# Kernel optimization log

Hardware: AMD Instinct MI355X
Metric: run time of the kernel (lower is better)

Reference implementation:

```python
import jax, jax.numpy as jnp
import numpy as np

POOL = 7
IMAGE_SHAPE = (1024, 1024, 3)


def _crop_and_resize(fmap, boxes, pool):
    """TF-style crop_and_resize with extrapolation_value=0.
    fmap: [C, H, W]; boxes: [N, (y1,x1,y2,x2)] normalized. Returns [N, C, pool, pool]."""
    C, H, W = fmap.shape
    dt = fmap.dtype
    y1, x1, y2, x2 = boxes[:, 0], boxes[:, 1], boxes[:, 2], boxes[:, 3]
    g = jnp.arange(pool, dtype=dt) / (pool - 1)  # [P] in [0,1]
    ys = (y1[:, None] + g[None, :] * (y2 - y1)[:, None]) * (H - 1)  # [N,P]
    xs = (x1[:, None] + g[None, :] * (x2 - x1)[:, None]) * (W - 1)  # [N,P]
    y0f = jnp.floor(ys); x0f = jnp.floor(xs)
    ly = (ys - y0f).astype(dt); lx = (xs - x0f).astype(dt)
    y0 = jnp.clip(y0f.astype(jnp.int32), 0, H - 1)
    y1i = jnp.clip(y0 + 1, 0, H - 1)
    x0 = jnp.clip(x0f.astype(jnp.int32), 0, W - 1)
    x1i = jnp.clip(x0 + 1, 0, W - 1)
    vy = ((ys >= 0) & (ys <= H - 1)).astype(dt)  # extrapolation_value = 0 outside
    vx = ((xs >= 0) & (xs <= W - 1)).astype(dt)

    def at(yi, xi):
        # gather -> [C, N, P, P]
        return fmap[:, yi[:, :, None], xi[:, None, :]]

    wy0 = (1 - ly)[None, :, :, None]; wy1 = ly[None, :, :, None]
    wx0 = (1 - lx)[None, :, None, :]; wx1 = lx[None, :, None, :]
    val = (at(y0, x0) * wy0 + at(y1i, x0) * wy1) * wx0 \
        + (at(y0, x1i) * wy0 + at(y1i, x1i) * wy1) * wx1
    val = val * (vy[None, :, :, None] * vx[None, :, None, :])
    return jnp.transpose(val, (1, 0, 2, 3))  # [N, C, P, P]


def reference(boxes, p2, p3, p4, p5):
    """pyramid_roi_align: route each box to FPN level 2..5 via the 224-scale
    log2 heuristic, then CropAndResize(pool, pool, 0) from that level.
    Output order matches input box order (original sorts back by box_to_level)."""
    h = boxes[:, 2] - boxes[:, 0]
    w = boxes[:, 3] - boxes[:, 1]
    image_area = float(IMAGE_SHAPE[0] * IMAGE_SHAPE[1])
    roi_level = 4.0 + jnp.log2(jnp.sqrt(h * w) / (224.0 / np.sqrt(image_area)))
    roi_level = jnp.clip(jnp.round(roi_level).astype(jnp.int32), 2, 5)
    boxes_d = jax.lax.stop_gradient(boxes)  # level_boxes.detach() in original
    fmaps = [p2, p3, p4, p5]
    pooled = jnp.zeros((boxes.shape[0], p2.shape[0], POOL, POOL), dtype=p2.dtype)
    for i, level in enumerate(range(2, 6)):
        mask = (roi_level == level).astype(p2.dtype)[:, None, None, None]
        pooled = pooled + mask * _crop_and_resize(fmaps[i], boxes_d, POOL)
    return pooled


def setup_inputs():
    key = jax.random.key(0)
    kb, ks, k2, k3, k4, k5 = jax.random.split(key, 6)
    N, C = 1000, 256
    size = jax.random.uniform(ks, (N, 2), minval=0.02, maxval=0.9)
    tl = jax.random.uniform(kb, (N, 2)) * (1.0 - size)  # top-left so box stays in [0,1]
    boxes = jnp.concatenate([tl[:, 0:1], tl[:, 1:2],
                             tl[:, 0:1] + size[:, 0:1], tl[:, 1:2] + size[:, 1:2]], axis=1)
    p2 = jax.random.normal(k2, (C, 256, 256), jnp.float32)
    p3 = jax.random.normal(k3, (C, 128, 128), jnp.float32)
    p4 = jax.random.normal(k4, (C, 64, 64), jnp.float32)
    p5 = jax.random.normal(k5, (C, 32, 32), jnp.float32)
    return {"boxes": boxes, "p2": p2, "p3": p3, "p4": p4, "p5": p5}
```

## Files before the change

kernel.cpp:

```cpp
#include <hip/hip_runtime.h>


#define POOL 7
#define NCH  256
#define ELEMS_PER_BOX (NCH * POOL * POOL)
#define ECH 32
#define WCH 16
#define SCH 4
#define NSTEPS 4
#define ROWS 14
#define MAXG 7
#define BUFSLOT (MAXG * 64)
#define STEPOUT (SCH * 49)

typedef float f2 __attribute__((ext_vector_type(2)));
typedef __attribute__((address_space(1))) const void* gas_ptr;
typedef __attribute__((address_space(3))) void*       las_ptr;

#define VMWAIT(n) asm volatile("s_waitcnt vmcnt(" #n ")" ::: "memory")

template<int S4S>
__device__ __forceinline__ void fast_steps(
    const float* __restrict__ lvl, float* __restrict__ opw,
    float* __restrict__ buf0, float* __restrict__ buf1,
    const int lane, const int HW, const unsigned cb0, const unsigned lim,
    const int xb0, const int* s_rowoff, const int* s_dx,
    const float* s_a, const float* s_b, const float* s_w0, const float* s_w1)
{
    constexpr int G   = (56 * S4S + 63) / 64;
    constexpr int S   = 4 * S4S;
    constexpr int NSL = 56 * S4S;

    unsigned inv0 = 0x40000000u, inv1 = 0x40000000u, inv2 = 0x40000000u,
             inv3 = 0x40000000u, inv4 = 0x40000000u, inv5 = 0x40000000u,
             inv6 = 0x40000000u;
#define SLOTMETA(k, var)                                                      \
    if constexpr ((k) < G) {                                                  \
        const int idx = (k) * 64 + lane;                                      \
        if (idx < NSL) {                                                      \
            const int rid = idx / S4S;                         \
            const int q   = idx - rid * S4S;                                  \
            const int cl  = rid / 14;                                         \
            const int r   = rid - 14 * cl;                                    \
            var = (unsigned)(cl * HW + s_rowoff[r] + xb0 + 4 * q);            \
        }                                                                     \
    }
    SLOTMETA(0, inv0) SLOTMETA(1, inv1) SLOTMETA(2, inv2) SLOTMETA(3, inv3)
    SLOTMETA(4, inv4) SLOTMETA(5, inv5) SLOTMETA(6, inv6)
#undef SLOTMETA

    int   to0, to1, to2, to3;
    float aa0, bb0, w00, w10, aa1, bb1, w01, w11;
    float aa2, bb2, w02, w12, aa3, bb3, w03, w13;
#define CELLMETA(j, tov, aav, bbv, w0v, w1v)                                  \
    { int oidx = (j) * 64 + lane;                                             \
      oidx = oidx < STEPOUT ? oidx : STEPOUT - 1;                             \
      const int cc = oidx / 49;                                               \
      const int pp = oidx - 49 * cc;                                          \
      tov = (cc * ROWS + 2 * (pp / 7)) * S + s_dx[pp];                        \
      aav = s_a[pp]; bbv = s_b[pp]; w0v = s_w0[pp]; w1v = s_w1[pp]; }
    CELLMETA(0, to0, aa0, bb0, w00, w10)
    CELLMETA(1, to1, aa1, bb1, w01, w11)
    CELLMETA(2, to2, aa2, bb2, w02, w12)
    CELLMETA(3, to3, aa3, bb3, w03, w13)
#undef CELLMETA

#define GLD1(k, var, so, bp)                                                  \
    if constexpr ((k) < G) {                                                  \
        unsigned o_ = (so) + var; o_ = o_ > lim ? lim : o_;                   \
        __builtin_amdgcn_global_load_lds((gas_ptr)(lvl + o_),                 \
            (las_ptr)((bp) + ((k) * 64 + lane) * 4), 16, 0, 0);               \
    }
#define ISSUE(t, bp)                                                          \
    { const unsigned so_ = cb0 + (unsigned)((t) * SCH * HW);                  \
      GLD1(0, inv0, so_, bp) GLD1(1, inv1, so_, bp) GLD1(2, inv2, so_, bp)    \
      GLD1(3, inv3, so_, bp) GLD1(4, inv4, so_, bp) GLD1(5, inv5, so_, bp)    \
      GLD1(6, inv6, so_, bp) }
#define CELLC(bp, tov, aav, bbv, w0v, w1v, rvar)                              \
    { const float t00 = (bp)[tov],     t01 = (bp)[tov + 1];                   \
      const float t10 = (bp)[tov + S], t11 = (bp)[tov + S + 1];               \
      rvar = (t00 * aav + t01 * bbv) * w0v + (t10 * aav + t11 * bbv) * w1v; }
#define VMWAIT_G                                                              \
    if constexpr (G == 1) { VMWAIT(1); }                                      \
    else if constexpr (G == 3) { VMWAIT(3); }                                 \
    else if constexpr (G == 5) { VMWAIT(5); }                                 \
    else { VMWAIT(7); }

    float r00, r01, r02, r03, r10, r11, r12, r13;
    float r20, r21, r22, r23, r30, r31, r32, r33;

    ISSUE(0, buf0)
    ISSUE(1, buf1)

    VMWAIT_G;
    __builtin_amdgcn_sched_barrier(0);
    CELLC(buf0, to0, aa0, bb0, w00, w10, r00)
    CELLC(buf0, to1, aa1, bb1, w01, w11, r01)
    CELLC(buf0, to2, aa2, bb2, w02, w12, r02)
    CELLC(buf0, to3, aa3, bb3, w03, w13, r03)
    asm volatile("s_waitcnt lgkmcnt(0)" ::: "memory");
    __builtin_amdgcn_sched_barrier(0);
    ISSUE(2, buf0)

    VMWAIT_G;
    __builtin_amdgcn_sched_barrier(0);
    CELLC(buf1, to0, aa0, bb0, w00, w10, r10)
    CELLC(buf1, to1, aa1, bb1, w01, w11, r11)
    CELLC(buf1, to2, aa2, bb2, w02, w12, r12)
    CELLC(buf1, to3, aa3, bb3, w03, w13, r13)
    asm volatile("s_waitcnt lgkmcnt(0)" ::: "memory");
    __builtin_amdgcn_sched_barrier(0);
    ISSUE(3, buf1)

    VMWAIT_G;
    __builtin_amdgcn_sched_barrier(0);
    CELLC(buf0, to0, aa0, bb0, w00, w10, r20)
    CELLC(buf0, to1, aa1, bb1, w01, w11, r21)
    CELLC(buf0, to2, aa2, bb2, w02, w12, r22)
    CELLC(buf0, to3, aa3, bb3, w03, w13, r23)

    VMWAIT(0);
    __builtin_amdgcn_sched_barrier(0);
    CELLC(buf1, to0, aa0, bb0, w00, w10, r30)
    CELLC(buf1, to1, aa1, bb1, w01, w11, r31)
    CELLC(buf1, to2, aa2, bb2, w02, w12, r32)
    CELLC(buf1, to3, aa3, bb3, w03, w13, r33)

    const bool tail = (lane < STEPOUT - 192);
    opw[0 * STEPOUT +   0 + lane] = r00;
    opw[0 * STEPOUT +  64 + lane] = r01;
    opw[0 * STEPOUT + 128 + lane] = r02;
    if (tail) opw[0 * STEPOUT + 192 + lane] = r03;
    opw[1 * STEPOUT +   0 + lane] = r10;
    opw[1 * STEPOUT +  64 + lane] = r11;
    opw[1 * STEPOUT + 128 + lane] = r12;
    if (tail) opw[1 * STEPOUT + 192 + lane] = r13;
    opw[2 * STEPOUT +   0 + lane] = r20;
    opw[2 * STEPOUT +  64 + lane] = r21;
    opw[2 * STEPOUT + 128 + lane] = r22;
    if (tail) opw[2 * STEPOUT + 192 + lane] = r23;
    opw[3 * STEPOUT +   0 + lane] = r30;
    opw[3 * STEPOUT +  64 + lane] = r31;
    opw[3 * STEPOUT + 128 + lane] = r32;
    if (tail) opw[3 * STEPOUT + 192 + lane] = r33;

#undef GLD1
#undef ISSUE
#undef CELLC
#undef VMWAIT_G
}

__global__ __launch_bounds__(128, 4) void roi_align_kernel(
    const float* __restrict__ boxes,
    const float* __restrict__ p2, const float* __restrict__ p3,
    const float* __restrict__ p4, const float* __restrict__ p5,
    float* __restrict__ out, int N)
{
    const int bid    = blockIdx.x;
    const int n      = bid >> 3;
    const int eighth = bid & 7;

    __shared__ float s_stage[2][2][BUFSLOT * 4];
    __shared__ float s_a[49], s_b[49], s_w0[49], s_w1[49];
    __shared__ int   s_dx[49];
    __shared__ int   s_off0[49], s_off1[49];
    __shared__ int   s_rowoff[ROWS];
    __shared__ int   s_HW, s_xb0, s_sel;
    __shared__ const float* s_fmap;

    const int tid = threadIdx.x;

    if (tid < 49) {
        const float by1 = boxes[4 * n + 0];
        const float bx1 = boxes[4 * n + 1];
        const float by2 = boxes[4 * n + 2];
        const float bx2 = boxes[4 * n + 3];
        const float h = by2 - by1;
        const float w = bx2 - bx1;
        float rl = 4.0f + log2f(sqrtf(h * w) / 0.21875f);
        int level = (int)rintf(rl);
        level = min(5, max(2, level));
        const int H = 256 >> (level - 2);
        const int W = H;
        const int py = tid / 7;
        const int px = tid - 7 * py;

        const float ty = (float)py / 6.0f;
        const float ys = (by1 + ty * (by2 - by1)) * (float)(H - 1);
        const float yf = floorf(ys);
        const float ly = ys - yf;
        int y0 = (int)yf; y0 = min(H - 1, max(0, y0));
        const int y1 = min(H - 1, y0 + 1);
        const float vy = (ys >= 0.0f && ys <= (float)(H - 1)) ? 1.0f : 0.0f;

        const float tx = (float)px / 6.0f;
        const float xs = (bx1 + tx * (bx2 - bx1)) * (float)(W - 1);
        const float xf = floorf(xs);
        const float lx = xs - xf;
        int x0 = (int)xf; x0 = min(W - 1, max(0, x0));
        const float vx = (xs >= 0.0f && xs <= (float)(W - 1)) ? 1.0f : 0.0f;
        const int xb = min(x0, W - 2);
        const bool edge = (x0 != xb);
        const float a = edge ? 0.0f : vx * (1.0f - lx);
        const float b = edge ? vx : vx * lx;

        const float xsA = bx1 * (float)(W - 1);
        int xA = (int)floorf(xsA); xA = min(W - 1, max(0, xA));
        const int xbA = min(xA, W - 2);
        const float xsB = bx2 * (float)(W - 1);
        int xB = (int)floorf(xsB); xB = min(W - 1, max(0, xB));
        const int xbB = min(xB, W - 2);
        const int xb0  = xbA & ~3;
        const int need = xbB + 2 - xb0;
        const int sa4  = (need + 3) >> 2;

        s_off0[tid] = y0 * W + xb;
        s_off1[tid] = y1 * W + xb;
        s_a[tid] = a;
        s_b[tid] = b;
        s_w0[tid] = vy * (1.0f - ly);
        s_w1[tid] = vy * ly;
        s_dx[tid] = xb - xb0;
        if (px == 0) {
            s_rowoff[2 * py]     = y0 * W;
            s_rowoff[2 * py + 1] = y1 * W;
        }
        if (tid == 0) {
            s_HW   = H * W;
            s_fmap = (level == 2) ? p2 : (level == 3) ? p3 : (level == 4) ? p4 : p5;
            s_xb0  = xb0;
            s_sel  = (need <= 28) ? (sa4 | 1) : 0;
        }
    }
    __syncthreads();

    const int HW = s_HW;
    const float* __restrict__ lvl = s_fmap;
    const int lane = tid & 63;
    const int wave = tid >> 6;
    const int sel  = s_sel;

    if (sel) {
        const int chw = eighth * ECH + wave * WCH;
        const unsigned cb0 = (unsigned)chw * (unsigned)HW;
        const unsigned lim = (unsigned)(NCH * HW - 4);
        float* buf0 = &s_stage[wave][0][0];
        float* buf1 = &s_stage[wave][1][0];
        float* __restrict__ opw =
            out + (size_t)n * ELEMS_PER_BOX + (size_t)chw * 49;

        if (sel == 3)
            fast_steps<3>(lvl, opw, buf0, buf1, lane, HW, cb0, lim, s_xb0,
                          s_rowoff, s_dx, s_a, s_b, s_w0, s_w1);
        else if (sel == 5)
            fast_steps<5>(lvl, opw, buf0, buf1, lane, HW, cb0, lim, s_xb0,
                          s_rowoff, s_dx, s_a, s_b, s_w0, s_w1);
        else if (sel == 7)
            fast_steps<7>(lvl, opw, buf0, buf1, lane, HW, cb0, lim, s_xb0,
                          s_rowoff, s_dx, s_a, s_b, s_w0, s_w1);
        else
            fast_steps<1>(lvl, opw, buf0, buf1, lane, HW, cb0, lim, s_xb0,
                          s_rowoff, s_dx, s_a, s_b, s_w0, s_w1);
    } else {
        const int c1  = tid / 49,  p1  = tid - 49 * c1;
        const int o2  = 128 + tid;
        const int o2c = o2 < STEPOUT ? o2 : STEPOUT - 1;
        const int c2  = o2c / 49,  p2i = o2c - 49 * c2;
        const bool act2 = (tid < STEPOUT - 128);

        const float a1 = s_a[p1],  b1 = s_b[p1],  w01f = s_w0[p1],  w11f = s_w1[p1];
        const float a2 = s_a[p2i], b2 = s_b[p2i], w02f = s_w0[p2i], w12f = s_w1[p2i];
        const int off01 = s_off0[p1],  off11 = s_off1[p1];
        const int off02 = s_off0[p2i], off12 = s_off1[p2i];

        const float* __restrict__ fbase = lvl + (size_t)(eighth * ECH) * HW;
        float* __restrict__ op =
            out + (size_t)n * ELEMS_PER_BOX + (size_t)(eighth * ECH) * 49;
        for (int g = 0; g < 8; ++g) {
            const float* pl1 = fbase + (size_t)(g * SCH + c1) * HW;
            const f2 q0 = *(const f2*)(pl1 + off01);
            const f2 q1 = *(const f2*)(pl1 + off11);
            const float r0 = q0.x * a1 + q0.y * b1;
            const float r1 = q1.x * a1 + q1.y * b1;
            op[g * STEPOUT + tid] = r0 * w01f + r1 * w11f;
            if (act2) {
                const float* pl2 = fbase + (size_t)(g * SCH + c2) * HW;
                const f2 u0 = *(const f2*)(pl2 + off02);
                const f2 u1 = *(const f2*)(pl2 + off12);
                const float s0 = u0.x * a2 + u0.y * b2;
                const float s1 = u1.x * a2 + u1.y * b2;
                op[g * STEPOUT + 128 + tid] = s0 * w02f + s1 * w12f;
            }
        }
    }
}

extern "C" void kernel_launch(void* const* d_in, const int* in_sizes, int n_in,
                              void* d_out, int out_size, void* d_ws, size_t ws_size,
                              hipStream_t stream) {
    const float* boxes = (const float*)d_in[0];
    const float* p2    = (const float*)d_in[1];
    const float* p3    = (const float*)d_in[2];
    const float* p4    = (const float*)d_in[3];
    const float* p5    = (const float*)d_in[4];
    float* out = (float*)d_out;
    const int N = in_sizes[0] / 4;

    roi_align_kernel<<<N * 8, 128, 0, stream>>>(boxes, p2, p3, p4, p5, out, N);
}
```

Before: 145.1 us.

## Split work into single-wave blocks of 16 channels with box-minor block ordering

Each block now runs one 64-thread wave covering 16 channels instead of two waves covering 32, so the grid doubles to N*16 blocks. Block index is decoded box-minor (n = bid % N), so consecutive blocks touch different boxes of the same channel slice. The slow path is rewritten to loop 13 times over a 784-output tile with incremental channel/pixel indexing and per-iteration LDS lookups. The aim is finer-grained scheduling and better load balance, at the cost of repeating the per-box setup (box decode, level selection, table building) twice as often and different L2 locality.

```diff
diff --git a/kernel.cpp b/kernel.cpp
--- a/kernel.cpp
+++ b/kernel.cpp
@@ -4,7 +4,6 @@
 #define POOL 7
 #define NCH  256
 #define ELEMS_PER_BOX (NCH * POOL * POOL)
-#define ECH 32
 #define WCH 16
 #define SCH 4
 #define NSTEPS 4
@@ -12,6 +11,7 @@
 #define MAXG 7
 #define BUFSLOT (MAXG * 64)
 #define STEPOUT (SCH * 49)
+#define BLKOUT (WCH * 49)
 
 typedef float f2 __attribute__((ext_vector_type(2)));
 typedef __attribute__((address_space(1))) const void* gas_ptr;
@@ -150,17 +150,17 @@
 #undef VMWAIT_G
 }
 
-__global__ __launch_bounds__(128, 4) void roi_align_kernel(
+__global__ __launch_bounds__(64, 2) void roi_align_kernel(
     const float* __restrict__ boxes,
     const float* __restrict__ p2, const float* __restrict__ p3,
     const float* __restrict__ p4, const float* __restrict__ p5,
     float* __restrict__ out, int N)
 {
-    const int bid    = blockIdx.x;
-    const int n      = bid >> 3;
-    const int eighth = bid & 7;
-
-    __shared__ float s_stage[2][2][BUFSLOT * 4];
+    const int bid       = blockIdx.x;
+    const int n         = bid % N;
+    const int sixteenth = bid / N;
+
+    __shared__ float s_stage[2][BUFSLOT * 4];
     __shared__ float s_a[49], s_b[49], s_w0[49], s_w1[49];
     __shared__ int   s_dx[49];
     __shared__ int   s_off0[49], s_off1[49];
@@ -236,61 +236,51 @@
 
     const int HW = s_HW;
     const float* __restrict__ lvl = s_fmap;
-    const int lane = tid & 63;
-    const int wave = tid >> 6;
+    const int lane = tid;
     const int sel  = s_sel;
+    const int chw  = sixteenth * WCH;
 
     if (sel) {
-        const int chw = eighth * ECH + wave * WCH;
         const unsigned cb0 = (unsigned)chw * (unsigned)HW;
         const unsigned lim = (unsigned)(NCH * HW - 4);
-        float* buf0 = &s_stage[wave][0][0];
-        float* buf1 = &s_stage[wave][1][0];
+        float* buf0 = &s_stage[0][0];
+        float* buf1 = &s_stage[1][0];
         float* __restrict__ opw =
             out + (size_t)n * ELEMS_PER_BOX + (size_t)chw * 49;
 
-        if (sel == 3)
-            fast_steps<3>(lvl, opw, buf0, buf1, lane, HW, cb0, lim, s_xb0,
-                          s_rowoff, s_dx, s_a, s_b, s_w0, s_w1);
-        else if (sel == 5)
+        if (sel == 5)
             fast_steps<5>(lvl, opw, buf0, buf1, lane, HW, cb0, lim, s_xb0,
                           s_rowoff, s_dx, s_a, s_b, s_w0, s_w1);
         else if (sel == 7)
             fast_steps<7>(lvl, opw, buf0, buf1, lane, HW, cb0, lim, s_xb0,
                           s_rowoff, s_dx, s_a, s_b, s_w0, s_w1);
+        else if (sel == 3)
+            fast_steps<3>(lvl, opw, buf0, buf1, lane, HW, cb0, lim, s_xb0,
+                          s_rowoff, s_dx, s_a, s_b, s_w0, s_w1);
         else
             fast_steps<1>(lvl, opw, buf0, buf1, lane, HW, cb0, lim, s_xb0,
                           s_rowoff, s_dx, s_a, s_b, s_w0, s_w1);
     } else {
-        const int c1  = tid / 49,  p1  = tid - 49 * c1;
-        const int o2  = 128 + tid;
-        const int o2c = o2 < STEPOUT ? o2 : STEPOUT - 1;
-        const int c2  = o2c / 49,  p2i = o2c - 49 * c2;
-        const bool act2 = (tid < STEPOUT - 128);
-
-        const float a1 = s_a[p1],  b1 = s_b[p1],  w01f = s_w0[p1],  w11f = s_w1[p1];
-        const float a2 = s_a[p2i], b2 = s_b[p2i], w02f = s_w0[p2i], w12f = s_w1[p2i];
-        const int off01 = s_off0[p1],  off11 = s_off1[p1];
-        const int off02 = s_off0[p2i], off12 = s_off1[p2i];
-
-        const float* __restrict__ fbase = lvl + (size_t)(eighth * ECH) * HW;
+        const float* __restrict__ fbase = lvl + (size_t)chw * HW;
         float* __restrict__ op =
-            out + (size_t)n * ELEMS_PER_BOX + (size_t)(eighth * ECH) * 49;
-        for (int g = 0; g < 8; ++g) {
-            const float* pl1 = fbase + (size_t)(g * SCH + c1) * HW;
-            const f2 q0 = *(const f2*)(pl1 + off01);
-            const f2 q1 = *(const f2*)(pl1 + off11);
-            const float r0 = q0.x * a1 + q0.y * b1;
-            const float r1 = q1.x * a1 + q1.y * b1;
-            op[g * STEPOUT + tid] = r0 * w01f + r1 * w11f;
-            if (act2) {
-                const float* pl2 = fbase + (size_t)(g * SCH + c2) * HW;
-                const f2 u0 = *(const f2*)(pl2 + off02);
-                const f2 u1 = *(const f2*)(pl2 + off12);
-                const float s0 = u0.x * a2 + u0.y * b2;
-                const float s1 = u1.x * a2 + u1.y * b2;
-                op[g * STEPOUT + 128 + tid] = s0 * w02f + s1 * w12f;
+            out + (size_t)n * ELEMS_PER_BOX + (size_t)chw * 49;
+
+        int c  = lane / 49;
+        int pp = lane - 49 * c;
+#pragma unroll
+        for (int g = 0; g < 13; ++g) {
+            const int o = g * 64 + lane;
+            if (g < 12 || lane < BLKOUT - 768) {
+                const float* pl = fbase + (size_t)c * HW;
+                const f2 q0 = *(const f2*)(pl + s_off0[pp]);
+                const f2 q1 = *(const f2*)(pl + s_off1[pp]);
+                const float aa = s_a[pp], bb = s_b[pp];
+                const float r0 = q0.x * aa + q0.y * bb;
+                const float r1 = q1.x * aa + q1.y * bb;
+                op[o] = r0 * s_w0[pp] + r1 * s_w1[pp];
             }
+            c += 1; pp += 15;
+            if (pp >= 49) { pp -= 49; c += 1; }
         }
     }
 }
@@ -306,5 +296,5 @@
     float* out = (float*)d_out;
     const int N = in_sizes[0] / 4;
 
-    roi_align_kernel<<<N * 8, 128, 0, stream>>>(boxes, p2, p3, p4, p5, out, N);
+    roi_align_kernel<<<N * 16, 64, 0, stream>>>(boxes, p2, p3, p4, p5, out, N);
 }
```

After: 149.3 us. 1.03x slower.
